# Kernel tuning notes

Hardware: AMD Instinct MI355X
Metric: run time of the kernel (lower is better)

## Reference

```python
import jax, jax.numpy as jnp
import numpy as np

B, CIN, H, W = 8, 1, 192, 192
COUT, KH, KW = 8, 7, 7


def setup_inputs() -> dict:
    key = jax.random.key(0)
    k1, k2, k3 = jax.random.split(key, 3)
    x = jax.random.normal(k1, (B, CIN, H, W), dtype=jnp.float32)
    # original init: filter ~ N(0, 0.01), alpha = 0 (use small nonzero alpha)
    filt = 0.01 * jax.random.normal(k2, (COUT, CIN, KH, KW), dtype=jnp.float32)
    alpha = 0.1 * jax.random.normal(k3, (COUT, CIN), dtype=jnp.float32)
    return {"x": x, "filt": filt, "alpha": alpha}


def _smorph(x, filt, alpha):
    # x: [B, Cin, H, W]; filt: [Cout, Cin, kh, kw]; alpha: [Cout, Cin]
    b, cin, h, w = x.shape
    cout, _, kh, kw = filt.shape
    ho, wo = h - kh + 1, w - kw + 1  # 'valid' windowing as in _smorph_py
    # sliding-window patches: [B, Cin, kh*kw, Ho, Wo] (static slices, traced once)
    patches = jnp.stack(
        [x[:, :, ky:ky + ho, kx:kx + wo] for ky in range(kh) for kx in range(kw)],
        axis=2,
    )
    # s[b,co,ci,k,y,x] = input[b,ci,y+ky,x+kx] + filter[co,ci,ky,kx]
    s = patches[:, None] + filt.reshape(cout, cin, kh * kw, 1, 1)[None]
    a = alpha[None, :, :, None, None, None]  # broadcast over B, taps, space
    e = jnp.exp(a * s)
    num = jnp.sum(s * e, axis=(2, 3))  # sum over Cin and taps -> [B,Cout,Ho,Wo]
    den = jnp.sum(e, axis=(2, 3))
    return num / den


def reference(x, filt, alpha):
    # dual=False: single soft-morphology pass
    return _smorph(x, filt, alpha)
```

## Files before the change

kernel.cpp:

```cpp
#include <hip/hip_runtime.h>

#ifndef __has_builtin
#define __has_builtin(x) 0
#endif

__device__ __forceinline__ float fexp2(float v) {
#if __has_builtin(__builtin_amdgcn_exp2f)
    return __builtin_amdgcn_exp2f(v);
#else
    return exp2f(v);
#endif
}
__device__ __forceinline__ float frcp(float v) {
#if __has_builtin(__builtin_amdgcn_rcpf)
    return __builtin_amdgcn_rcpf(v);
#else
    return 1.0f / v;
#endif
}

constexpr int B_    = 8;
constexpr int H_    = 192;
constexpr int W_    = 192;
constexpr int COUT_ = 8;
constexpr int KH_   = 7;
constexpr int KW_   = 7;
constexpr int HO_   = H_ - KH_ + 1;
constexpr int WO_   = W_ - KW_ + 1;
constexpr float LOG2E = 1.44269504088896340736f;

constexpr int TX   = 64;
constexpr int TY   = 8;
constexpr int IX   = TX + KW_ - 1;
constexpr int IY   = TY + KH_ - 1;
constexpr int NPIX = IX * IY;

__global__ void smorph_setup(const float* __restrict__ filt,
                             const float* __restrict__ alpha,
                             float* __restrict__ ws) {
    for (int i = threadIdx.x; i < COUT_ * KH_ * KW_; i += 256) {
        int c = i / 49, r = i - c * 49, ky = r / 7, kx = r - ky * 7;
        float a2 = alpha[c] * LOG2E;
        float f  = filt[c * 49 + ky * 7 + kx];
        float F  = fexp2(a2 * f);
        ws[c * 56 + ky * 8 + kx]       = F;
        ws[448 + c * 56 + ky * 8 + kx] = F * f;
    }
}

__global__ __launch_bounds__(256) void smorph_main(
    const float* __restrict__ x,
    const float* __restrict__ alpha,
    const float* __restrict__ fg,
    float* __restrict__ out)
{
    __shared__ __align__(16) float2 PH[IY * IX];

    const int tx = threadIdx.x;
    const int ty = threadIdx.y;
    const int tid = ty * 32 + tx;
    const int bx0 = blockIdx.x * TX;
    const int by0 = blockIdx.y * TY;
    const int b   = blockIdx.z;

    const float* xb = x + b * (H_ * W_);
    const float* sptr[4];
    int sidx[4];
    int scnt = 0;
    for (int i = tid; i < NPIX; i += 256) {
        int iy = i / IX, ix = i - iy * IX;
        int gy = min(by0 + iy, H_ - 1);
        int gx = min(bx0 + ix, W_ - 1);
        sptr[scnt] = xb + gy * W_ + gx;
        sidx[scnt] = i;
        ++scnt;
    }

    const int ox = bx0 + 2 * tx;
    const int oy = by0 + ty;
    const bool valid = (ox + 1 < WO_) && (oy < HO_);

#pragma unroll 1
    for (int c = 0; c < COUT_; ++c) {
        const float a2 = alpha[c] * LOG2E;

        for (int j = 0; j < scnt; ++j) {
            float xv = *sptr[j];
            float P  = fexp2(a2 * xv);
            PH[sidx[j]] = make_float2(P, xv * P);
        }
        __syncthreads();

        float num0 = 0.f, den0 = 0.f, num1 = 0.f, den1 = 0.f;
#pragma unroll
        for (int ky = 0; ky < KH_; ++ky) {
            float Fk[7], Gk[7];
#pragma unroll
            for (int j = 0; j < 7; ++j) {
                Fk[j] = fg[c * 56 + ky * 8 + j];
                Gk[j] = fg[448 + c * 56 + ky * 8 + j];
            }
            const float4* rp = (const float4*)&PH[(ty + ky) * IX + 2 * tx];
            float4 q0 = rp[0], q1 = rp[1], q2 = rp[2], q3 = rp[3];
            float P[8] = {q0.x, q0.z, q1.x, q1.z, q2.x, q2.z, q3.x, q3.z};
            float Hh[8] = {q0.y, q0.w, q1.y, q1.w, q2.y, q2.w, q3.y, q3.w};
#pragma unroll
            for (int kx = 0; kx < 7; ++kx) {
                num0 = fmaf(Fk[kx], Hh[kx], num0);
                num0 = fmaf(Gk[kx], P[kx], num0);
                den0 = fmaf(Fk[kx], P[kx], den0);
                num1 = fmaf(Fk[kx], Hh[kx + 1], num1);
                num1 = fmaf(Gk[kx], P[kx + 1], num1);
                den1 = fmaf(Fk[kx], P[kx + 1], den1);
            }
        }

        if (valid) {
            float2 o;
            o.x = num0 * frcp(den0);
            o.y = num1 * frcp(den1);
            *(float2*)&out[((b * COUT_ + c) * HO_ + oy) * WO_ + ox] = o;
        }
        __syncthreads();
    }
}

extern "C" void kernel_launch(void* const* d_in, const int* in_sizes, int n_in,
                              void* d_out, int out_size, void* d_ws, size_t ws_size,
                              hipStream_t stream) {
    const float* x     = (const float*)d_in[0];
    const float* filt  = (const float*)d_in[1];
    const float* alpha = (const float*)d_in[2];
    float* out = (float*)d_out;
    float* ws  = (float*)d_ws;

    smorph_setup<<<1, 256, 0, stream>>>(filt, alpha, ws);

    dim3 block(32, 8, 1);
    dim3 grid((WO_ + TX - 1) / TX, (HO_ + TY - 1) / TY, B_);
    smorph_main<<<grid, block, 0, stream>>>(x, alpha, ws, out);
}
```

Measured before the change: 86.18 us.

## Double-buffer shared tile per channel, cache input in registers, repack filter table

The shared exp tile is now double-buffered across output channels, which removes the trailing barrier in each channel iteration. Input pixels are loaded once into registers instead of being re-read from global memory for every channel. The filter table is repacked so each row's F and F*f values sit contiguously (16 floats per row), and the setup kernel now uses 64 threads. Shared memory use doubles, which may reduce occupancy.

Result: faster. 81.93 us (-4.9%).

```diff
diff --git a/kernel.cpp b/kernel.cpp
--- a/kernel.cpp
+++ b/kernel.cpp
@@ -38,13 +38,19 @@
 __global__ void smorph_setup(const float* __restrict__ filt,
                              const float* __restrict__ alpha,
                              float* __restrict__ ws) {
-    for (int i = threadIdx.x; i < COUT_ * KH_ * KW_; i += 256) {
-        int c = i / 49, r = i - c * 49, ky = r / 7, kx = r - ky * 7;
+    int i = threadIdx.x;
+    if (i < COUT_ * KH_) {
+        int c = i / 7, ky = i - c * 7;
         float a2 = alpha[c] * LOG2E;
-        float f  = filt[c * 49 + ky * 7 + kx];
-        float F  = fexp2(a2 * f);
-        ws[c * 56 + ky * 8 + kx]       = F;
-        ws[448 + c * 56 + ky * 8 + kx] = F * f;
+        float* t = ws + (c * 7 + ky) * 16;
+#pragma unroll
+        for (int kx = 0; kx < 7; ++kx) {
+            float f = filt[(c * 7 + ky) * 7 + kx];
+            float F = fexp2(a2 * f);
+            t[kx]     = F;
+            t[8 + kx] = F * f;
+        }
+        t[7] = 0.f; t[15] = 0.f;
     }
 }
 
@@ -54,27 +60,27 @@
     const float* __restrict__ fg,
     float* __restrict__ out)
 {
-    __shared__ __align__(16) float2 PH[IY * IX];
+    __shared__ __align__(16) float2 PH[2][IY * IX];
 
-    const int tx = threadIdx.x;
-    const int ty = threadIdx.y;
+    const int tx  = threadIdx.x;
+    const int ty  = threadIdx.y;
     const int tid = ty * 32 + tx;
     const int bx0 = blockIdx.x * TX;
     const int by0 = blockIdx.y * TY;
     const int b   = blockIdx.z;
+    const float* xb = x + b * (H_ * W_);
 
-    const float* xb = x + b * (H_ * W_);
-    const float* sptr[4];
-    int sidx[4];
-    int scnt = 0;
-    for (int i = tid; i < NPIX; i += 256) {
-        int iy = i / IX, ix = i - iy * IX;
-        int gy = min(by0 + iy, H_ - 1);
-        int gx = min(bx0 + ix, W_ - 1);
-        sptr[scnt] = xb + gy * W_ + gx;
-        sidx[scnt] = i;
-        ++scnt;
-    }
+    const int i0 = tid, i1 = tid + 256, i2 = tid + 512, i3 = tid + 768;
+    const int iy0 = i0 / IX, ix0 = i0 - iy0 * IX;
+    const int iy1 = i1 / IX, ix1 = i1 - iy1 * IX;
+    const int iy2 = i2 / IX, ix2 = i2 - iy2 * IX;
+    const int iy3 = i3 / IX, ix3 = i3 - iy3 * IX;
+    const bool has3 = (i3 < NPIX);
+
+    const float xv0 = xb[min(by0 + iy0, H_ - 1) * W_ + min(bx0 + ix0, W_ - 1)];
+    const float xv1 = xb[min(by0 + iy1, H_ - 1) * W_ + min(bx0 + ix1, W_ - 1)];
+    const float xv2 = xb[min(by0 + iy2, H_ - 1) * W_ + min(bx0 + ix2, W_ - 1)];
+    const float xv3 = has3 ? xb[min(by0 + iy3, H_ - 1) * W_ + min(bx0 + ix3, W_ - 1)] : 0.f;
 
     const int ox = bx0 + 2 * tx;
     const int oy = by0 + ty;
@@ -82,36 +88,36 @@
 
 #pragma unroll 1
     for (int c = 0; c < COUT_; ++c) {
+        float2* cur = PH[c & 1];
         const float a2 = alpha[c] * LOG2E;
 
-        for (int j = 0; j < scnt; ++j) {
-            float xv = *sptr[j];
-            float P  = fexp2(a2 * xv);
-            PH[sidx[j]] = make_float2(P, xv * P);
+        {
+            float P;
+            P = fexp2(a2 * xv0); cur[iy0 * IX + ix0] = make_float2(P, xv0 * P);
+            P = fexp2(a2 * xv1); cur[iy1 * IX + ix1] = make_float2(P, xv1 * P);
+            P = fexp2(a2 * xv2); cur[iy2 * IX + ix2] = make_float2(P, xv2 * P);
+            if (has3) { P = fexp2(a2 * xv3); cur[iy3 * IX + ix3] = make_float2(P, xv3 * P); }
         }
         __syncthreads();
 
         float num0 = 0.f, den0 = 0.f, num1 = 0.f, den1 = 0.f;
+        const float* tc = fg + c * (7 * 16);
 #pragma unroll
         for (int ky = 0; ky < KH_; ++ky) {
-            float Fk[7], Gk[7];
-#pragma unroll
-            for (int j = 0; j < 7; ++j) {
-                Fk[j] = fg[c * 56 + ky * 8 + j];
-                Gk[j] = fg[448 + c * 56 + ky * 8 + j];
-            }
-            const float4* rp = (const float4*)&PH[(ty + ky) * IX + 2 * tx];
+            const float* t = tc + ky * 16;
+            const float4* rp = (const float4*)&cur[(ty + ky) * IX + 2 * tx];
             float4 q0 = rp[0], q1 = rp[1], q2 = rp[2], q3 = rp[3];
-            float P[8] = {q0.x, q0.z, q1.x, q1.z, q2.x, q2.z, q3.x, q3.z};
+            float P[8]  = {q0.x, q0.z, q1.x, q1.z, q2.x, q2.z, q3.x, q3.z};
             float Hh[8] = {q0.y, q0.w, q1.y, q1.w, q2.y, q2.w, q3.y, q3.w};
 #pragma unroll
             for (int kx = 0; kx < 7; ++kx) {
-                num0 = fmaf(Fk[kx], Hh[kx], num0);
-                num0 = fmaf(Gk[kx], P[kx], num0);
-                den0 = fmaf(Fk[kx], P[kx], den0);
-                num1 = fmaf(Fk[kx], Hh[kx + 1], num1);
-                num1 = fmaf(Gk[kx], P[kx + 1], num1);
-                den1 = fmaf(Fk[kx], P[kx + 1], den1);
+                const float F = t[kx], G = t[8 + kx];
+                num0 = fmaf(F, Hh[kx],     num0);
+                num0 = fmaf(G, P[kx],      num0);
+                den0 = fmaf(F, P[kx],      den0);
+                num1 = fmaf(F, Hh[kx + 1], num1);
+                num1 = fmaf(G, P[kx + 1],  num1);
+                den1 = fmaf(F, P[kx + 1],  den1);
             }
         }
 
@@ -121,7 +127,6 @@
             o.y = num1 * frcp(den1);
             *(float2*)&out[((b * COUT_ + c) * HO_ + oy) * WO_ + ox] = o;
         }
-        __syncthreads();
     }
 }
 
@@ -134,7 +139,7 @@
     float* out = (float*)d_out;
     float* ws  = (float*)d_ws;
 
-    smorph_setup<<<1, 256, 0, stream>>>(filt, alpha, ws);
+    smorph_setup<<<1, 64, 0, stream>>>(filt, alpha, ws);
 
     dim3 block(32, 8, 1);
     dim3 grid((WO_ + TX - 1) / TX, (HO_ + TY - 1) / TY, B_);
```
